# Kernel optimization log

Measured on AMD Instinct MI355X. Metric: run time of the kernel, lower is better.

The kernel has to match this reference:

```python
import jax, jax.numpy as jnp
import numpy as np

N = 100000
E = 3200000
IN_C = 128
HID = 16
OUT_C = 16
EA = 16


def setup_inputs() -> dict:
    key = jax.random.key(0)
    ks = jax.random.split(key, 8)
    x = jax.random.normal(ks[0], (N, IN_C), dtype=jnp.float32)
    edge_index = jax.random.randint(ks[1], (2, E), 0, N, dtype=jnp.int32)
    edge_attr = jax.random.normal(ks[2], (E, EA), dtype=jnp.float32)
    We = jax.random.normal(ks[3], (EA, HID), dtype=jnp.float32) * (1.0 / np.sqrt(EA))
    be = jnp.zeros((HID,), dtype=jnp.float32)
    W1 = jax.random.normal(ks[4], (IN_C, HID), dtype=jnp.float32) * (1.0 / np.sqrt(IN_C))
    b1 = jnp.zeros((HID,), dtype=jnp.float32)
    W2 = jax.random.normal(ks[5], (HID, OUT_C), dtype=jnp.float32) * (1.0 / np.sqrt(HID))
    b2 = jnp.zeros((OUT_C,), dtype=jnp.float32)
    return {"x": x, "edge_index": edge_index, "edge_attr": edge_attr,
            "We": We, "be": be, "W1": W1, "b1": b1, "W2": W2, "b2": b2}


def _gcn_conv(h, src, dst, ew, dinv_src, dinv_dst, dinv_sq, W, b):
    # h: [N, Cin] -> transform first (PyG order), then normalized gather-scatter.
    h = h @ W                                   # [N, C], C == HID == OUT_C == 16
    norm = dinv_src * ew * dinv_dst             # [E, 16] per-edge per-channel norm
    msg = norm * h[src]                          # gather + fuse edge weight
    agg = jax.ops.segment_sum(msg, dst, num_segments=N)  # scatter-add
    agg = agg + dinv_sq * h                      # self-loop (weight 1) contribution
    return agg + b


def reference(x, edge_index, edge_attr, We, be, W1, b1, W2, b2):
    src, dst = edge_index[0], edge_index[1]
    ew = edge_attr @ We + be                     # [E, 16] edge weights (per channel)
    # symmetric degree normalization with self loops (weight 1), per channel
    deg = jax.ops.segment_sum(ew, dst, num_segments=N) + 1.0  # [N, 16]
    dinv = jnp.where(deg > 0, jax.lax.rsqrt(jnp.abs(deg) + 1e-12), 0.0)
    dinv_src = dinv[src]
    dinv_dst = dinv[dst]
    dinv_sq = dinv * dinv
    h = jax.nn.relu(_gcn_conv(x, src, dst, ew, dinv_src, dinv_dst, dinv_sq, W1, b1))
    # dropout is identity in eval mode
    out = _gcn_conv(h, src, dst, ew, dinv_src, dinv_dst, dinv_sq, W2, b2)
    return out
```

## Files before the change

kernel.cpp:

```cpp
#include <hip/hip_runtime.h>

static constexpr int N_NODES = 100000;
static constexpr int N_EDGES = 3200000;
static constexpr int NC16    = N_NODES * 16;
static constexpr int RB      = 256;
static constexpr int NB      = (N_NODES + RB - 1) / RB;
static constexpr int CAP     = 9000;
static constexpr int EPB     = 8192;
static constexpr int NPB     = (N_EDGES + EPB - 1) / EPB;

__device__ __forceinline__ float4 v4fma(float s, float4 w, float4 acc) {
    acc.x = fmaf(s, w.x, acc.x);
    acc.y = fmaf(s, w.y, acc.y);
    acc.z = fmaf(s, w.z, acc.z);
    acc.w = fmaf(s, w.w, acc.w);
    return acc;
}

template<int KK>
__device__ __forceinline__ float4 qbcast(float4 a) {
    constexpr int ctrl = KK * 0x55;
    float4 r;
    r.x = __int_as_float(__builtin_amdgcn_mov_dpp(__float_as_int(a.x), ctrl, 0xF, 0xF, true));
    r.y = __int_as_float(__builtin_amdgcn_mov_dpp(__float_as_int(a.y), ctrl, 0xF, 0xF, true));
    r.z = __int_as_float(__builtin_amdgcn_mov_dpp(__float_as_int(a.z), ctrl, 0xF, 0xF, true));
    r.w = __int_as_float(__builtin_amdgcn_mov_dpp(__float_as_int(a.w), ctrl, 0xF, 0xF, true));
    return r;
}

template<int KK>
__device__ __forceinline__ float4 ewstep(float4 a, const float4* wc, float4 ew) {
    float4 v = qbcast<KK>(a);
    ew = v4fma(v.x, wc[4*KK + 0], ew);
    ew = v4fma(v.y, wc[4*KK + 1], ew);
    ew = v4fma(v.z, wc[4*KK + 2], ew);
    ew = v4fma(v.w, wc[4*KK + 3], ew);
    return ew;
}

__global__ __launch_bounds__(256)
void k_zero(int* g) {
    int t = blockIdx.x * 256 + threadIdx.x;
    if (t < NB) g[t] = 0;
}

__global__ __launch_bounds__(512)
void k_part_ew(const int* __restrict__ srcI, const int* __restrict__ dstI,
               const float* __restrict__ ea, const float* __restrict__ We,
               const float* __restrict__ be,
               int* __restrict__ gcount,
               float4* __restrict__ ewRec4, int* __restrict__ metaRec)
{
    __shared__ int hist[NB];
    const int tid  = threadIdx.x;
    const int e0   = blockIdx.x * EPB;
    const int ecnt = min(EPB, N_EDGES - e0);
    for (int t = tid; t < NB; t += 512) hist[t] = 0;
    __syncthreads();
    for (int i = tid; i < ecnt; i += 512) {
        int d = dstI[e0 + i];
        atomicAdd(&hist[d >> 8], 1);
    }
    __syncthreads();
    for (int t = tid; t < NB; t += 512) {
        int h = hist[t];
        hist[t] = (h > 0) ? atomicAdd(&gcount[t], h) : 0;
    }
    __syncthreads();

    const int c4 = tid & 3;
    float4 wc[16];
    const float4* We4 = (const float4*)We;
#pragma unroll
    for (int k = 0; k < 16; ++k) wc[k] = We4[k * 4 + c4];
    const float4 bev = ((const float4*)be)[c4];
    const float4* ea4 = (const float4*)ea;

    for (int i = tid >> 2; i < ecnt; i += 128) {
        const int e = e0 + i;
        const int d = dstI[e];
        const int s = srcI[e];
        const int b = d >> 8;
        float4 a = ea4[e * 4 + c4];
        float4 ew = bev;
        ew = ewstep<0>(a, wc, ew);
        ew = ewstep<1>(a, wc, ew);
        ew = ewstep<2>(a, wc, ew);
        ew = ewstep<3>(a, wc, ew);
        int pos = 0;
        if (c4 == 0) pos = atomicAdd(&hist[b], 1);
        pos = __shfl(pos, (threadIdx.x & 63) & ~3, 64);
        if (pos < CAP) {
            const int r = b * CAP + pos;
            ewRec4[r * 4 + c4] = ew;
            if (c4 == 0) metaRec[r] = (s << 8) | (d & 255);
        }
    }
}

__global__ __launch_bounds__(512)
void k_degdinv(const float4* __restrict__ ewRec4, const int* __restrict__ metaRec,
               const int* __restrict__ gcount, float* __restrict__ dinv)
{
    __shared__ double accS[RB * 16];
    const int tid = threadIdx.x;
    const int b   = blockIdx.x;
    for (int t = tid; t < RB * 16; t += 512) accS[t] = 0.0;
    const int c4  = tid & 3;
    const int cnt = min(gcount[b], CAP);
    const int base = b * CAP;
    __syncthreads();

#pragma unroll 2
    for (int i = tid >> 2; i < cnt; i += 128) {
        float4 ew = ewRec4[(base + i) * 4 + c4];
        int m = metaRec[base + i];
        int dl = m & 255;
        double* o = accS + dl * 16 + c4 * 4;
        atomicAdd(o + 0, (double)ew.x);
        atomicAdd(o + 1, (double)ew.y);
        atomicAdd(o + 2, (double)ew.z);
        atomicAdd(o + 3, (double)ew.w);
    }
    __syncthreads();

    for (int t = tid; t < RB * 4; t += 512) {
        int nl = t >> 2;
        int ng = b * RB + nl;
        if (ng < N_NODES) {
            const double* s = accS + nl * 16 + (t & 3) * 4;
            float4 o;
            float d0 = (float)s[0] + 1.0f; o.x = (d0 > 0.f) ? rsqrtf(d0 + 1e-12f) : 0.f;
            float d1 = (float)s[1] + 1.0f; o.y = (d1 > 0.f) ? rsqrtf(d1 + 1e-12f) : 0.f;
            float d2 = (float)s[2] + 1.0f; o.z = (d2 > 0.f) ? rsqrtf(d2 + 1e-12f) : 0.f;
            float d3 = (float)s[3] + 1.0f; o.w = (d3 > 0.f) ? rsqrtf(d3 + 1e-12f) : 0.f;
            ((float4*)dinv)[ng * 4 + (t & 3)] = o;
        }
    }
}

__global__ __launch_bounds__(512)
void k_gather(const float4* __restrict__ ewRec4, const int* __restrict__ metaRec,
              const int* __restrict__ gcount, const float* __restrict__ p,
              float* __restrict__ acc)
{
    __shared__ double accS[RB * 16];
    const int tid = threadIdx.x;
    const int b   = blockIdx.x;
    for (int t = tid; t < RB * 16; t += 512) accS[t] = 0.0;
    const int c4  = tid & 3;
    const int cnt = min(gcount[b], CAP);
    const int base = b * CAP;
    const float4* p4 = (const float4*)p;
    __syncthreads();

#pragma unroll 2
    for (int i = tid >> 2; i < cnt; i += 128) {
        float4 ew = ewRec4[(base + i) * 4 + c4];
        int m = metaRec[base + i];
        float4 pv = p4[((unsigned)m >> 8) * 4 + c4];
        int dl = m & 255;
        double* o = accS + dl * 16 + c4 * 4;
        atomicAdd(o + 0, (double)(ew.x * pv.x));
        atomicAdd(o + 1, (double)(ew.y * pv.y));
        atomicAdd(o + 2, (double)(ew.z * pv.z));
        atomicAdd(o + 3, (double)(ew.w * pv.w));
    }
    __syncthreads();

    for (int t = tid; t < RB * 4; t += 512) {
        int nl = t >> 2;
        int ng = b * RB + nl;
        if (ng < N_NODES) {
            const double* s = accS + nl * 16 + (t & 3) * 4;
            float4 o;
            o.x = (float)s[0]; o.y = (float)s[1];
            o.z = (float)s[2]; o.w = (float)s[3];
            ((float4*)acc)[ng * 4 + (t & 3)] = o;
        }
    }
}

__global__ __launch_bounds__(256)
void k_part(const int* __restrict__ srcI, const int* __restrict__ dstI,
            int* __restrict__ gcount, int2* __restrict__ meta)
{
    __shared__ int hist[NB];
    const int tid  = threadIdx.x;
    const int e0   = blockIdx.x * EPB;
    const int ecnt = min(EPB, N_EDGES - e0);
    for (int t = tid; t < NB; t += 256) hist[t] = 0;
    __syncthreads();
    for (int i = tid; i < ecnt; i += 256) {
        int d = dstI[e0 + i];
        atomicAdd(&hist[d >> 8], 1);
    }
    __syncthreads();
    for (int t = tid; t < NB; t += 256) {
        int h = hist[t];
        hist[t] = (h > 0) ? atomicAdd(&gcount[t], h) : 0;
    }
    __syncthreads();
    for (int i = tid; i < ecnt; i += 256) {
        int e = e0 + i;
        int d = dstI[e];
        int s = srcI[e];
        int b = d >> 8;
        int pos = atomicAdd(&hist[b], 1);
        if (pos < CAP)
            meta[b * CAP + pos] = make_int2(e, (s << 8) | (d & 255));
    }
}

template<bool HAS_P>
__global__ __launch_bounds__(512)
void k_bucket(const float* __restrict__ ea, const int2* __restrict__ meta,
              const int* __restrict__ gcount, const float* __restrict__ We,
              const float* __restrict__ be, const float* __restrict__ p,
              float* __restrict__ acc)
{
    __shared__ double accS[RB * 16];
    const int tid = threadIdx.x;
    const int b   = blockIdx.x;
    for (int t = tid; t < RB * 16; t += 512) accS[t] = 0.0;

    const int c4 = tid & 3;
    float4 wc[16];
    const float4* We4 = (const float4*)We;
#pragma unroll
    for (int k = 0; k < 16; ++k) wc[k] = We4[k * 4 + c4];
    const float4 bev = ((const float4*)be)[c4];
    const int cnt = min(gcount[b], CAP);
    const int2* ml = meta + b * CAP;
    const float4* ea4 = (const float4*)ea;
    const float4* p4  = (const float4*)p;
    __syncthreads();

#pragma unroll 2
    for (int i = tid >> 2; i < cnt; i += 128) {
        int2 m = ml[i];
        float4 a = ea4[m.x * 4 + c4];
        float4 pv;
        if (HAS_P) pv = p4[((unsigned)m.y >> 8) * 4 + c4];
        const int dl = m.y & 255;
        float4 ew = bev;
        ew = ewstep<0>(a, wc, ew);
        ew = ewstep<1>(a, wc, ew);
        ew = ewstep<2>(a, wc, ew);
        ew = ewstep<3>(a, wc, ew);
        double* o = accS + dl * 16 + c4 * 4;
        if (HAS_P) {
            atomicAdd(o + 0, (double)(ew.x * pv.x));
            atomicAdd(o + 1, (double)(ew.y * pv.y));
            atomicAdd(o + 2, (double)(ew.z * pv.z));
            atomicAdd(o + 3, (double)(ew.w * pv.w));
        } else {
            atomicAdd(o + 0, (double)ew.x);
            atomicAdd(o + 1, (double)ew.y);
            atomicAdd(o + 2, (double)ew.z);
            atomicAdd(o + 3, (double)ew.w);
        }
    }
    __syncthreads();

    for (int t = tid; t < RB * 4; t += 512) {
        int nl = t >> 2;
        int ng = b * RB + nl;
        if (ng < N_NODES) {
            const double* s = accS + nl * 16 + (t & 3) * 4;
            float4 o;
            o.x = (float)s[0]; o.y = (float)s[1];
            o.z = (float)s[2]; o.w = (float)s[3];
            ((float4*)acc)[ng * 4 + (t & 3)] = o;
        }
    }
}

__global__ __launch_bounds__(256)
void k_dinv(float* dd) {
    int t = blockIdx.x * 256 + threadIdx.x;
    if (t < NC16) {
        float d = dd[t] + 1.0f;
        dd[t] = (d > 0.0f) ? rsqrtf(d + 1e-12f) : 0.0f;
    }
}

__global__ __launch_bounds__(256)
void k_xw1(const float* __restrict__ x, const float* __restrict__ W1,
           const float* __restrict__ dinv, float* __restrict__ p)
{
    __shared__ float4 w1s[512];
    const int t = threadIdx.x;
    const float4* W14 = (const float4*)W1;
    w1s[t]       = W14[t];
    w1s[t + 256] = W14[t + 256];
    __syncthreads();

    const int c4 = t & 3;
    const int nl = t >> 2;
    const int nb = blockIdx.x * 256;
    int node[4];
    float4 acc[4];
#pragma unroll
    for (int i = 0; i < 4; ++i) {
        node[i] = nb + i * 64 + nl;
        acc[i]  = make_float4(0.f, 0.f, 0.f, 0.f);
    }
    const float4* x4 = (const float4*)x;

    for (int k4 = 0; k4 < 32; ++k4) {
        float4 wv0 = w1s[(k4 * 4 + 0) * 4 + c4];
        float4 wv1 = w1s[(k4 * 4 + 1) * 4 + c4];
        float4 wv2 = w1s[(k4 * 4 + 2) * 4 + c4];
        float4 wv3 = w1s[(k4 * 4 + 3) * 4 + c4];
#pragma unroll
        for (int i = 0; i < 4; ++i) {
            int nn = node[i] < N_NODES ? node[i] : (N_NODES - 1);
            float4 xv = x4[nn * 32 + k4];
            acc[i] = v4fma(xv.x, wv0, acc[i]);
            acc[i] = v4fma(xv.y, wv1, acc[i]);
            acc[i] = v4fma(xv.z, wv2, acc[i]);
            acc[i] = v4fma(xv.w, wv3, acc[i]);
        }
    }
    const float4* dinv4 = (const float4*)dinv;
    float4* pp = (float4*)p;
#pragma unroll
    for (int i = 0; i < 4; ++i) {
        if (node[i] < N_NODES) {
            float4 dv = dinv4[node[i] * 4 + c4];
            float4 o;
            o.x = dv.x * acc[i].x; o.y = dv.y * acc[i].y;
            o.z = dv.z * acc[i].z; o.w = dv.w * acc[i].w;
            pp[node[i] * 4 + c4] = o;
        }
    }
}

__global__ __launch_bounds__(256)
void k_mid(const float* __restrict__ accA, const float* __restrict__ dinv,
           const float* __restrict__ W2, const float* __restrict__ b1,
           float* __restrict__ p)
{
    const int tid = blockIdx.x * 256 + threadIdx.x;
    const int q   = tid >> 2;
    if (q >= N_NODES) return;
    const int c4 = threadIdx.x & 3;

    float4 wc[16];
    const float4* W24 = (const float4*)W2;
#pragma unroll
    for (int k = 0; k < 16; ++k) wc[k] = W24[k * 4 + c4];
    const float4 b1v = ((const float4*)b1)[c4];

    const float4 av = ((const float4*)accA)[q * 4 + c4];
    const float4 pv = ((const float4*)p)[q * 4 + c4];
    const float4 dv = ((const float4*)dinv)[q * 4 + c4];

    float4 h1;
    h1.x = fmaxf(fmaf(dv.x, av.x + pv.x, b1v.x), 0.f);
    h1.y = fmaxf(fmaf(dv.y, av.y + pv.y, b1v.y), 0.f);
    h1.z = fmaxf(fmaf(dv.z, av.z + pv.z, b1v.z), 0.f);
    h1.w = fmaxf(fmaf(dv.w, av.w + pv.w, b1v.w), 0.f);

    float4 h2 = make_float4(0.f, 0.f, 0.f, 0.f);
    h2 = ewstep<0>(h1, wc, h2);
    h2 = ewstep<1>(h1, wc, h2);
    h2 = ewstep<2>(h1, wc, h2);
    h2 = ewstep<3>(h1, wc, h2);

    float4 o;
    o.x = dv.x * h2.x; o.y = dv.y * h2.y;
    o.z = dv.z * h2.z; o.w = dv.w * h2.w;
    ((float4*)p)[q * 4 + c4] = o;
}

__global__ __launch_bounds__(256)
void k_out(const float* __restrict__ accB, const float* __restrict__ dinv,
           const float* __restrict__ p, const float* __restrict__ b2,
           float* __restrict__ out)
{
    const int tid = blockIdx.x * 256 + threadIdx.x;
    const int q   = tid >> 2;
    if (q >= N_NODES) return;
    const int c4 = threadIdx.x & 3;
    const float4 b2v = ((const float4*)b2)[c4];
    const float4 av = ((const float4*)accB)[q * 4 + c4];
    const float4 pv = ((const float4*)p)[q * 4 + c4];
    const float4 dv = ((const float4*)dinv)[q * 4 + c4];
    float4 o;
    o.x = fmaf(dv.x, av.x + pv.x, b2v.x);
    o.y = fmaf(dv.y, av.y + pv.y, b2v.y);
    o.z = fmaf(dv.z, av.z + pv.z, b2v.z);
    o.w = fmaf(dv.w, av.w + pv.w, b2v.w);
    ((float4*)out)[q * 4 + c4] = o;
}

extern "C" void kernel_launch(void* const* d_in, const int* in_sizes, int n_in,
                              void* d_out, int out_size, void* d_ws, size_t ws_size,
                              hipStream_t stream)
{
    const float* x   = (const float*)d_in[0];
    const int*   ei  = (const int*)d_in[1];
    const float* ea  = (const float*)d_in[2];
    const float* We  = (const float*)d_in[3];
    const float* be  = (const float*)d_in[4];
    const float* W1  = (const float*)d_in[5];
    const float* b1  = (const float*)d_in[6];
    const float* W2  = (const float*)d_in[7];
    const float* b2  = (const float*)d_in[8];
    float* out = (float*)d_out;

    const int* srcI = ei;
    const int* dstI = ei + N_EDGES;

    float* dinv = (float*)d_ws;
    float* p    = dinv + NC16;
    float* accA = p + NC16;
    float* accB = accA + NC16;

    const size_t needA = (size_t)4 * NC16 * 4
                       + (size_t)NB * CAP * (sizeof(float4) * 4 + sizeof(int))
                       + (size_t)NB * sizeof(int) + 4096;

    const dim3 blk(256);

    if (ws_size >= needA) {
        float4* ewRec4 = (float4*)(accB + NC16);
        int*    metaRec = (int*)(ewRec4 + (size_t)NB * CAP * 4);
        int*    gcount  = metaRec + (size_t)NB * CAP;

        hipLaunchKernelGGL(k_zero, dim3((NB + 255) / 256), blk, 0, stream, gcount);
        hipLaunchKernelGGL(k_part_ew, dim3(NPB), dim3(512), 0, stream,
                           srcI, dstI, ea, We, be, gcount, ewRec4, metaRec);
        hipLaunchKernelGGL(k_degdinv, dim3(NB), dim3(512), 0, stream,
                           ewRec4, metaRec, gcount, dinv);
        hipLaunchKernelGGL(k_xw1, dim3((N_NODES + 255) / 256), blk, 0, stream,
                           x, W1, dinv, p);
        hipLaunchKernelGGL(k_gather, dim3(NB), dim3(512), 0, stream,
                           ewRec4, metaRec, gcount, p, accA);
        hipLaunchKernelGGL(k_mid, dim3((N_NODES * 4 + 255) / 256), blk, 0, stream,
                           accA, dinv, W2, b1, p);
        hipLaunchKernelGGL(k_gather, dim3(NB), dim3(512), 0, stream,
                           ewRec4, metaRec, gcount, p, accB);
        hipLaunchKernelGGL(k_out, dim3((N_NODES * 4 + 255) / 256), blk, 0, stream,
                           accB, dinv, p, b2, out);
    } else {
        int2* meta   = (int2*)(accB + NC16);
        int*  gcount = (int*)(meta + (size_t)NB * CAP);

        hipLaunchKernelGGL(k_zero, dim3((NB + 255) / 256), blk, 0, stream, gcount);
        hipLaunchKernelGGL(k_part, dim3(NPB), blk, 0, stream, srcI, dstI, gcount, meta);
        hipLaunchKernelGGL((k_bucket<false>), dim3(NB), dim3(512), 0, stream,
                           ea, meta, gcount, We, be, (const float*)nullptr, dinv);
        hipLaunchKernelGGL(k_dinv, dim3(NC16 / 256), blk, 0, stream, dinv);
        hipLaunchKernelGGL(k_xw1, dim3((N_NODES + 255) / 256), blk, 0, stream,
                           x, W1, dinv, p);
        hipLaunchKernelGGL((k_bucket<true>), dim3(NB), dim3(512), 0, stream,
                           ea, meta, gcount, We, be, p, accA);
        hipLaunchKernelGGL(k_mid, dim3((N_NODES * 4 + 255) / 256), blk, 0, stream,
                           accA, dinv, W2, b1, p);
        hipLaunchKernelGGL((k_bucket<true>), dim3(NB), dim3(512), 0, stream,
                           ea, meta, gcount, We, be, p, accB);
        hipLaunchKernelGGL(k_out, dim3((N_NODES * 4 + 255) / 256), blk, 0, stream,
                           accB, dinv, p, b2, out);
    }
}
```

Before: 693.2 us.

## Halve destination bucket size, use 1024-thread blocks, and swizzle LDS accumulator columns

Shrinks each destination bucket from 256 to 128 nodes, which doubles the bucket count and lowers CAP. Blocks grow to 1024 threads, and partitioning now uses a fixed 512 blocks. A per-row rotation of the 16 double accumulators in shared memory is meant to spread the 4-lane atomic groups across LDS banks and reduce conflicts. The intent is more parallel blocks in the gather/scatter passes and less LDS contention. The risks are more global atomics on gcount, lower occupancy per CU with 1024-thread blocks, and the tighter CAP of 4800 per 128-node bucket (about 4100 edges expected), which could overflow and silently drop edges.

Result: faster. 651.4 us (-6.0%).

```diff
diff --git a/kernel.cpp b/kernel.cpp
--- a/kernel.cpp
+++ b/kernel.cpp
@@ -3,11 +3,11 @@
 static constexpr int N_NODES = 100000;
 static constexpr int N_EDGES = 3200000;
 static constexpr int NC16    = N_NODES * 16;
-static constexpr int RB      = 256;
+static constexpr int RB      = 128;
 static constexpr int NB      = (N_NODES + RB - 1) / RB;
-static constexpr int CAP     = 9000;
-static constexpr int EPB     = 8192;
-static constexpr int NPB     = (N_EDGES + EPB - 1) / EPB;
+static constexpr int CAP     = 4800;
+static constexpr int NPB     = 512;
+static constexpr int EPB     = (N_EDGES + NPB - 1) / NPB;
 
 __device__ __forceinline__ float4 v4fma(float s, float4 w, float4 acc) {
     acc.x = fmaf(s, w.x, acc.x);
@@ -38,13 +38,23 @@
     return ew;
 }
 
+__device__ __forceinline__ void accum4(double* __restrict__ accS, int dl, int c4,
+                                       double v0, double v1, double v2, double v3) {
+    double* row = accS + dl * 16;
+    const int pb = (c4 * 4 + dl) & 15;
+    atomicAdd(row + ((pb + 0) & 15), v0);
+    atomicAdd(row + ((pb + 1) & 15), v1);
+    atomicAdd(row + ((pb + 2) & 15), v2);
+    atomicAdd(row + ((pb + 3) & 15), v3);
+}
+
 __global__ __launch_bounds__(256)
 void k_zero(int* g) {
     int t = blockIdx.x * 256 + threadIdx.x;
     if (t < NB) g[t] = 0;
 }
 
-__global__ __launch_bounds__(512)
+__global__ __launch_bounds__(1024)
 void k_part_ew(const int* __restrict__ srcI, const int* __restrict__ dstI,
                const float* __restrict__ ea, const float* __restrict__ We,
                const float* __restrict__ be,
@@ -55,14 +65,14 @@
     const int tid  = threadIdx.x;
     const int e0   = blockIdx.x * EPB;
     const int ecnt = min(EPB, N_EDGES - e0);
-    for (int t = tid; t < NB; t += 512) hist[t] = 0;
-    __syncthreads();
-    for (int i = tid; i < ecnt; i += 512) {
+    for (int t = tid; t < NB; t += 1024) hist[t] = 0;
+    __syncthreads();
+    for (int i = tid; i < ecnt; i += 1024) {
         int d = dstI[e0 + i];
-        atomicAdd(&hist[d >> 8], 1);
-    }
-    __syncthreads();
-    for (int t = tid; t < NB; t += 512) {
+        atomicAdd(&hist[d >> 7], 1);
+    }
+    __syncthreads();
+    for (int t = tid; t < NB; t += 1024) {
         int h = hist[t];
         hist[t] = (h > 0) ? atomicAdd(&gcount[t], h) : 0;
     }
@@ -76,11 +86,11 @@
     const float4 bev = ((const float4*)be)[c4];
     const float4* ea4 = (const float4*)ea;
 
-    for (int i = tid >> 2; i < ecnt; i += 128) {
+    for (int i = tid >> 2; i < ecnt; i += 256) {
         const int e = e0 + i;
         const int d = dstI[e];
         const int s = srcI[e];
-        const int b = d >> 8;
+        const int b = d >> 7;
         float4 a = ea4[e * 4 + c4];
         float4 ew = bev;
         ew = ewstep<0>(a, wc, ew);
@@ -93,53 +103,50 @@
         if (pos < CAP) {
             const int r = b * CAP + pos;
             ewRec4[r * 4 + c4] = ew;
-            if (c4 == 0) metaRec[r] = (s << 8) | (d & 255);
-        }
-    }
-}
-
-__global__ __launch_bounds__(512)
+            if (c4 == 0) metaRec[r] = (s << 7) | (d & 127);
+        }
+    }
+}
+
+__global__ __launch_bounds__(1024)
 void k_degdinv(const float4* __restrict__ ewRec4, const int* __restrict__ metaRec,
                const int* __restrict__ gcount, float* __restrict__ dinv)
 {
     __shared__ double accS[RB * 16];
     const int tid = threadIdx.x;
     const int b   = blockIdx.x;
-    for (int t = tid; t < RB * 16; t += 512) accS[t] = 0.0;
+    for (int t = tid; t < RB * 16; t += 1024) accS[t] = 0.0;
     const int c4  = tid & 3;
     const int cnt = min(gcount[b], CAP);
     const int base = b * CAP;
     __syncthreads();
 
 #pragma unroll 2
-    for (int i = tid >> 2; i < cnt; i += 128) {
+    for (int i = tid >> 2; i < cnt; i += 256) {
         float4 ew = ewRec4[(base + i) * 4 + c4];
         int m = metaRec[base + i];
-        int dl = m & 255;
-        double* o = accS + dl * 16 + c4 * 4;
-        atomicAdd(o + 0, (double)ew.x);
-        atomicAdd(o + 1, (double)ew.y);
-        atomicAdd(o + 2, (double)ew.z);
-        atomicAdd(o + 3, (double)ew.w);
-    }
-    __syncthreads();
-
-    for (int t = tid; t < RB * 4; t += 512) {
+        int dl = m & 127;
+        accum4(accS, dl, c4, (double)ew.x, (double)ew.y, (double)ew.z, (double)ew.w);
+    }
+    __syncthreads();
+
+    for (int t = tid; t < RB * 4; t += 1024) {
         int nl = t >> 2;
         int ng = b * RB + nl;
         if (ng < N_NODES) {
-            const double* s = accS + nl * 16 + (t & 3) * 4;
+            const double* s = accS + nl * 16;
+            const int pb = ((t & 3) * 4 + nl) & 15;
             float4 o;
-            float d0 = (float)s[0] + 1.0f; o.x = (d0 > 0.f) ? rsqrtf(d0 + 1e-12f) : 0.f;
-            float d1 = (float)s[1] + 1.0f; o.y = (d1 > 0.f) ? rsqrtf(d1 + 1e-12f) : 0.f;
-            float d2 = (float)s[2] + 1.0f; o.z = (d2 > 0.f) ? rsqrtf(d2 + 1e-12f) : 0.f;
-            float d3 = (float)s[3] + 1.0f; o.w = (d3 > 0.f) ? rsqrtf(d3 + 1e-12f) : 0.f;
+            float d0 = (float)s[(pb + 0) & 15] + 1.0f; o.x = (d0 > 0.f) ? rsqrtf(d0 + 1e-12f) : 0.f;
+            float d1 = (float)s[(pb + 1) & 15] + 1.0f; o.y = (d1 > 0.f) ? rsqrtf(d1 + 1e-12f) : 0.f;
+            float d2 = (float)s[(pb + 2) & 15] + 1.0f; o.z = (d2 > 0.f) ? rsqrtf(d2 + 1e-12f) : 0.f;
+            float d3 = (float)s[(pb + 3) & 15] + 1.0f; o.w = (d3 > 0.f) ? rsqrtf(d3 + 1e-12f) : 0.f;
             ((float4*)dinv)[ng * 4 + (t & 3)] = o;
         }
     }
 }
 
-__global__ __launch_bounds__(512)
+__global__ __launch_bounds__(1024)
 void k_gather(const float4* __restrict__ ewRec4, const int* __restrict__ metaRec,
               const int* __restrict__ gcount, const float* __restrict__ p,
               float* __restrict__ acc)
@@ -147,7 +154,7 @@
     __shared__ double accS[RB * 16];
     const int tid = threadIdx.x;
     const int b   = blockIdx.x;
-    for (int t = tid; t < RB * 16; t += 512) accS[t] = 0.0;
+    for (int t = tid; t < RB * 16; t += 1024) accS[t] = 0.0;
     const int c4  = tid & 3;
     const int cnt = min(gcount[b], CAP);
     const int base = b * CAP;
@@ -155,33 +162,34 @@
     __syncthreads();
 
 #pragma unroll 2
-    for (int i = tid >> 2; i < cnt; i += 128) {
+    for (int i = tid >> 2; i < cnt; i += 256) {
         float4 ew = ewRec4[(base + i) * 4 + c4];
         int m = metaRec[base + i];
-        float4 pv = p4[((unsigned)m >> 8) * 4 + c4];
-        int dl = m & 255;
-        double* o = accS + dl * 16 + c4 * 4;
-        atomicAdd(o + 0, (double)(ew.x * pv.x));
-        atomicAdd(o + 1, (double)(ew.y * pv.y));
-        atomicAdd(o + 2, (double)(ew.z * pv.z));
-        atomicAdd(o + 3, (double)(ew.w * pv.w));
-    }
-    __syncthreads();
-
-    for (int t = tid; t < RB * 4; t += 512) {
+        float4 pv = p4[((unsigned)m >> 7) * 4 + c4];
+        int dl = m & 127;
+        accum4(accS, dl, c4,
+               (double)(ew.x * pv.x), (double)(ew.y * pv.y),
+               (double)(ew.z * pv.z), (double)(ew.w * pv.w));
+    }
+    __syncthreads();
+
+    for (int t = tid; t < RB * 4; t += 1024) {
         int nl = t >> 2;
         int ng = b * RB + nl;
         if (ng < N_NODES) {
-            const double* s = accS + nl * 16 + (t & 3) * 4;
+            const double* s = accS + nl * 16;
+            const int pb = ((t & 3) * 4 + nl) & 15;
             float4 o;
-            o.x = (float)s[0]; o.y = (float)s[1];
-            o.z = (float)s[2]; o.w = (float)s[3];
+            o.x = (float)s[(pb + 0) & 15];
+            o.y = (float)s[(pb + 1) & 15];
+            o.z = (float)s[(pb + 2) & 15];
+            o.w = (float)s[(pb + 3) & 15];
             ((float4*)acc)[ng * 4 + (t & 3)] = o;
         }
     }
 }
 
-__global__ __launch_bounds__(256)
+__global__ __launch_bounds__(1024)
 void k_part(const int* __restrict__ srcI, const int* __restrict__ dstI,
             int* __restrict__ gcount, int2* __restrict__ meta)
 {
@@ -189,31 +197,31 @@
     const int tid  = threadIdx.x;
     const int e0   = blockIdx.x * EPB;
     const int ecnt = min(EPB, N_EDGES - e0);
-    for (int t = tid; t < NB; t += 256) hist[t] = 0;
-    __syncthreads();
-    for (int i = tid; i < ecnt; i += 256) {
+    for (int t = tid; t < NB; t += 1024) hist[t] = 0;
+    __syncthreads();
+    for (int i = tid; i < ecnt; i += 1024) {
         int d = dstI[e0 + i];
-        atomicAdd(&hist[d >> 8], 1);
-    }
-    __syncthreads();
-    for (int t = tid; t < NB; t += 256) {
+        atomicAdd(&hist[d >> 7], 1);
+    }
+    __syncthreads();
+    for (int t = tid; t < NB; t += 1024) {
         int h = hist[t];
         hist[t] = (h > 0) ? atomicAdd(&gcount[t], h) : 0;
     }
     __syncthreads();
-    for (int i = tid; i < ecnt; i += 256) {
+    for (int i = tid; i < ecnt; i += 1024) {
         int e = e0 + i;
         int d = dstI[e];
         int s = srcI[e];
-        int b = d >> 8;
+        int b = d >> 7;
         int pos = atomicAdd(&hist[b], 1);
         if (pos < CAP)
-            meta[b * CAP + pos] = make_int2(e, (s << 8) | (d & 255));
+            meta[b * CAP + pos] = make_int2(e, (s << 7) | (d & 127));
     }
 }
 
 template<bool HAS_P>
-__global__ __launch_bounds__(512)
+__global__ __launch_bounds__(1024)
 void k_bucket(const float* __restrict__ ea, const int2* __restrict__ meta,
               const int* __restrict__ gcount, const float* __restrict__ We,
               const float* __restrict__ be, const float* __restrict__ p,
@@ -222,7 +230,7 @@
     __shared__ double accS[RB * 16];
     const int tid = threadIdx.x;
     const int b   = blockIdx.x;
-    for (int t = tid; t < RB * 16; t += 512) accS[t] = 0.0;
+    for (int t = tid; t < RB * 16; t += 1024) accS[t] = 0.0;
 
     const int c4 = tid & 3;
     float4 wc[16];
@@ -237,40 +245,38 @@
     __syncthreads();
 
 #pragma unroll 2
-    for (int i = tid >> 2; i < cnt; i += 128) {
+    for (int i = tid >> 2; i < cnt; i += 256) {
         int2 m = ml[i];
         float4 a = ea4[m.x * 4 + c4];
         float4 pv;
-        if (HAS_P) pv = p4[((unsigned)m.y >> 8) * 4 + c4];
-        const int dl = m.y & 255;
+        if (HAS_P) pv = p4[((unsigned)m.y >> 7) * 4 + c4];
+        const int dl = m.y & 127;
         float4 ew = bev;
         ew = ewstep<0>(a, wc, ew);
         ew = ewstep<1>(a, wc, ew);
         ew = ewstep<2>(a, wc, ew);
         ew = ewstep<3>(a, wc, ew);
-        double* o = accS + dl * 16 + c4 * 4;
         if (HAS_P) {
-            atomicAdd(o + 0, (double)(ew.x * pv.x));
-            atomicAdd(o + 1, (double)(ew.y * pv.y));
-            atomicAdd(o + 2, (double)(ew.z * pv.z));
-            atomicAdd(o + 3, (double)(ew.w * pv.w));
+            accum4(accS, dl, c4,
+                   (double)(ew.x * pv.x), (double)(ew.y * pv.y),
+                   (double)(ew.z * pv.z), (double)(ew.w * pv.w));
         } else {
-            atomicAdd(o + 0, (double)ew.x);
-            atomicAdd(o + 1, (double)ew.y);
-            atomicAdd(o + 2, (double)ew.z);
-            atomicAdd(o + 3, (double)ew.w);
-        }
-    }
-    __syncthreads();
-
-    for (int t = tid; t < RB * 4; t += 512) {
+            accum4(accS, dl, c4, (double)ew.x, (double)ew.y, (double)ew.z, (double)ew.w);
+        }
+    }
+    __syncthreads();
+
+    for (int t = tid; t < RB * 4; t += 1024) {
         int nl = t >> 2;
         int ng = b * RB + nl;
         if (ng < N_NODES) {
-            const double* s = accS + nl * 16 + (t & 3) * 4;
+            const double* s = accS + nl * 16;
+            const int pb = ((t & 3) * 4 + nl) & 15;
             float4 o;
-            o.x = (float)s[0]; o.y = (float)s[1];
-            o.z = (float)s[2]; o.w = (float)s[3];
+            o.x = (float)s[(pb + 0) & 15];
+            o.y = (float)s[(pb + 1) & 15];
+            o.z = (float)s[(pb + 2) & 15];
+            o.w = (float)s[(pb + 3) & 15];
             ((float4*)acc)[ng * 4 + (t & 3)] = o;
         }
     }
@@ -431,17 +437,17 @@
         int*    gcount  = metaRec + (size_t)NB * CAP;
 
         hipLaunchKernelGGL(k_zero, dim3((NB + 255) / 256), blk, 0, stream, gcount);
-        hipLaunchKernelGGL(k_part_ew, dim3(NPB), dim3(512), 0, stream,
+        hipLaunchKernelGGL(k_part_ew, dim3(NPB), dim3(1024), 0, stream,
                            srcI, dstI, ea, We, be, gcount, ewRec4, metaRec);
-        hipLaunchKernelGGL(k_degdinv, dim3(NB), dim3(512), 0, stream,
+        hipLaunchKernelGGL(k_degdinv, dim3(NB), dim3(1024), 0, stream,
                            ewRec4, metaRec, gcount, dinv);
         hipLaunchKernelGGL(k_xw1, dim3((N_NODES + 255) / 256), blk, 0, stream,
                            x, W1, dinv, p);
-        hipLaunchKernelGGL(k_gather, dim3(NB), dim3(512), 0, stream,
+        hipLaunchKernelGGL(k_gather, dim3(NB), dim3(1024), 0, stream,
                            ewRec4, metaRec, gcount, p, accA);
         hipLaunchKernelGGL(k_mid, dim3((N_NODES * 4 + 255) / 256), blk, 0, stream,
                            accA, dinv, W2, b1, p);
-        hipLaunchKernelGGL(k_gather, dim3(NB), dim3(512), 0, stream,
+        hipLaunchKernelGGL(k_gather, dim3(NB), dim3(1024), 0, stream,
                            ewRec4, metaRec, gcount, p, accB);
         hipLaunchKernelGGL(k_out, dim3((N_NODES * 4 + 255) / 256), blk, 0, stream,
                            accB, dinv, p, b2, out);
@@ -450,17 +456,18 @@
         int*  gcount = (int*)(meta + (size_t)NB * CAP);
 
         hipLaunchKernelGGL(k_zero, dim3((NB + 255) / 256), blk, 0, stream, gcount);
-        hipLaunchKernelGGL(k_part, dim3(NPB), blk, 0, stream, srcI, dstI, gcount, meta);
-        hipLaunchKernelGGL((k_bucket<false>), dim3(NB), dim3(512), 0, stream,
+        hipLaunchKernelGGL(k_part, dim3(NPB), dim3(1024), 0, stream,
+                           srcI, dstI, gcount, meta);
+        hipLaunchKernelGGL((k_bucket<false>), dim3(NB), dim3(1024), 0, stream,
                            ea, meta, gcount, We, be, (const float*)nullptr, dinv);
         hipLaunchKernelGGL(k_dinv, dim3(NC16 / 256), blk, 0, stream, dinv);
         hipLaunchKernelGGL(k_xw1, dim3((N_NODES + 255) / 256), blk, 0, stream,
                            x, W1, dinv, p);
-        hipLaunchKernelGGL((k_bucket<true>), dim3(NB), dim3(512), 0, stream,
+        hipLaunchKernelGGL((k_bucket<true>), dim3(NB), dim3(1024), 0, stream,
                            ea, meta, gcount, We, be, p, accA);
         hipLaunchKernelGGL(k_mid, dim3((N_NODES * 4 + 255) / 256), blk, 0, stream,
                            accA, dinv, W2, b1, p);
-        hipLaunchKernelGGL((k_bucket<true>), dim3(NB), dim3(512), 0, stream,
+        hipLaunchKernelGGL((k_bucket<true>), dim3(NB), dim3(1024), 0, stream,
                            ea, meta, gcount, We, be, p, accB);
         hipLaunchKernelGGL(k_out, dim3((N_NODES * 4 + 255) / 256), blk, 0, stream,
                            accB, dinv, p, b2, out);
```
